# Kernel optimization log

Measured on AMD Instinct MI355X. Metric: run time of the kernel, lower is better.

The kernel has to match this reference:

```python
import jax, jax.numpy as jnp
import numpy as np

B, T, V, H, L = 32, 256, 32000, 512, 2

def setup_inputs() -> dict:
    key = jax.random.key(0)
    ks = jax.random.split(key, 6)
    scale = 1.0 / np.sqrt(H)
    tokens = jax.random.randint(ks[0], (B, T), 0, V)
    lengths = jax.random.randint(ks[1], (B,), T // 2, T + 1)
    embedding = jax.random.normal(ks[2], (V, H), jnp.float32) * scale
    Wx = jax.random.normal(ks[3], (L, H, 4 * H), jnp.float32) * scale
    Wh = jax.random.normal(ks[4], (L, H, 4 * H), jnp.float32) * scale
    b = jnp.zeros((L, 4 * H), jnp.float32)
    return {"tokens": tokens, "lengths": lengths, "embedding": embedding,
            "Wx": Wx, "Wh": Wh, "b": b}

def _lstm_layer(x, lengths, Wx, Wh, b):
    # x: [B, T, H]; length-masked carry (state frozen once t >= length)
    Bb, Tt, Hh = x.shape
    def step(carry, inp):
        c, h = carry
        xt, t = inp
        z = xt @ Wx + h @ Wh + b            # [B, 4H]
        i, f, g, o = jnp.split(z, 4, axis=-1)
        nc = jax.nn.sigmoid(f) * c + jax.nn.sigmoid(i) * jnp.tanh(g)
        nh = jax.nn.sigmoid(o) * jnp.tanh(nc)
        mask = (t < lengths)[:, None]
        c = jnp.where(mask, nc, c)
        h = jnp.where(mask, nh, h)
        return (c, h), h
    init = (jnp.zeros((Bb, Hh), x.dtype), jnp.zeros((Bb, Hh), x.dtype))
    (c, h), ys = jax.lax.scan(step, init, (jnp.swapaxes(x, 0, 1), jnp.arange(Tt)))
    return jnp.swapaxes(ys, 0, 1), (c, h)  # [B, T, H], ([B,H],[B,H])

def reference(tokens, lengths, embedding, Wx, Wh, b):
    x = embedding[tokens]                    # [B, T, H]
    final = None
    for l in range(Wx.shape[0]):             # small fixed layer loop
        x, final = _lstm_layer(x, lengths, Wx[l], Wh[l], b[l])
    # encoder returns (all outputs of top layer, final state of top layer)
    return x, final
```

## Files before the change

kernel.cpp:

```cpp
#include <hip/hip_runtime.h>

#define BB 32
#define TT 256
#define HH 512
#define NBLK 64
#define ALD 1032
#define ZLD 68
#define FLGSTRIDE 32

typedef float    f32x4 __attribute__((ext_vector_type(4)));
typedef float    f32x2 __attribute__((ext_vector_type(2)));
typedef int      i32x4 __attribute__((ext_vector_type(4)));
typedef _Float16 f16x8 __attribute__((ext_vector_type(8)));
typedef unsigned long long u64;

__device__ __forceinline__ unsigned short f2h(float f) {
  union { _Float16 h; unsigned short u; } v; v.h = (_Float16)f; return v.u;
}
__device__ __forceinline__ int pkh2(float a, float b) {
  return (int)((unsigned int)f2h(a) | ((unsigned int)f2h(b) << 16));
}
__device__ __forceinline__ float sigm(float x) { return 1.f / (1.f + __expf(-x)); }
__device__ __forceinline__ float tanh_(float x) {
  float ax = fabsf(x);
  float e = __expf(-2.f * ax);
  float r = (1.f - e) / (1.f + e);
  return copysignf(r, x);
}
__device__ __forceinline__ void ld_coh16(i32x4& dst, const void* a) {
  asm volatile("global_load_dwordx4 %0, %1, off sc1"
               : "=v"(dst) : "v"(a) : "memory");
}

__global__ void zero_ws_kernel(unsigned int* p, int nwords) {
  int i = blockIdx.x * 256 + threadIdx.x;
  if (i < nwords) p[i] = 0u;
}

__global__ __launch_bounds__(256, 1) void lstm_enc_kernel(
    const int* __restrict__ tokens,
    const int* __restrict__ lengths,
    const float* __restrict__ emb,
    const float* __restrict__ Wx,
    const float* __restrict__ Wh,
    const float* __restrict__ bias,
    float* __restrict__ out,
    unsigned short* __restrict__ ws_y,
    u64* __restrict__ htag,
    unsigned int* __restrict__ flags)
{
  const int tid   = threadIdx.x;
  const int blk   = blockIdx.x;
  const int layer = blk >> 5;
  const int lblk  = blk & 31;
  const int wave  = tid >> 6;
  const int lane  = tid & 63;

  __shared__ unsigned short Alds[32 * ALD];
  __shared__ float zlds[32 * ZLD];

  const int nloc  = lane & 15;
  const int gcol  = wave * HH + lblk * 16 + nloc;
  const int krow0 = (lane >> 4) * 8;
  const float* WxL = Wx + (size_t)layer * HH * 2048;
  const float* WhL = Wh + (size_t)layer * HH * 2048;
  f16x8 breg[32];
#pragma unroll
  for (int s = 0; s < 32; ++s) {
    const float* base = (s < 16)
        ? (WxL + (size_t)(s * 32 + krow0) * 2048 + gcol)
        : (WhL + (size_t)((s - 16) * 32 + krow0) * 2048 + gcol);
    f16x8 v;
    v[0] = (_Float16)base[0 * 2048];
    v[1] = (_Float16)base[1 * 2048];
    v[2] = (_Float16)base[2 * 2048];
    v[3] = (_Float16)base[3 * 2048];
    v[4] = (_Float16)base[4 * 2048];
    v[5] = (_Float16)base[5 * 2048];
    v[6] = (_Float16)base[6 * 2048];
    v[7] = (_Float16)base[7 * 2048];
    breg[s] = v;
  }

  const int jj  = tid & 7;
  const int eb  = tid >> 3;
  const int u0  = lblk * 16 + 2 * jj;
  const int len = lengths[eb];
  const float bI0 = bias[layer * 2048 +         u0], bI1 = bias[layer * 2048 +         u0 + 1];
  const float bF0 = bias[layer * 2048 +  512 +  u0], bF1 = bias[layer * 2048 +  512 +  u0 + 1];
  const float bG0 = bias[layer * 2048 + 1024 +  u0], bG1 = bias[layer * 2048 + 1024 +  u0 + 1];
  const float bO0 = bias[layer * 2048 + 1536 +  u0], bO1 = bias[layer * 2048 + 1536 +  u0 + 1];
  float cA = 0.f, hA = 0.f, cB = 0.f, hB = 0.f;

  u64* hlay = htag + (size_t)layer * 2 * BB * 256;
  unsigned int* pollL0 = flags + (size_t)(tid & 31) * FLGSTRIDE;

  if (layer == 0) {
#pragma unroll
    for (int i = 0; i < 8; ++i) {
      int u   = tid + i * 256;
      int row = u >> 6;
      int ce  = (u & 63) * 8;
      int tok = tokens[row * TT + 0];
      const float* src = emb + (size_t)tok * HH + ce;
      f32x4 lo = *(const f32x4*)src;
      f32x4 hi = *(const f32x4*)(src + 4);
      i32x4 w;
      w[0] = pkh2(lo[0], lo[1]); w[1] = pkh2(lo[2], lo[3]);
      w[2] = pkh2(hi[0], hi[1]); w[3] = pkh2(hi[2], hi[3]);
      *(i32x4*)(&Alds[row * ALD + ce]) = w;
    }
  }

  for (int it = 0;; ++it) {
    const int t = (layer == 0) ? it : (it - 1);
    const bool active = (t >= 0) && (t < TT);

    if (layer == 1 && active) {
      const unsigned int tgt = (unsigned int)(t + 1);
      if (tid < 32) {
        while (__hip_atomic_load(pollL0, __ATOMIC_RELAXED, __HIP_MEMORY_SCOPE_AGENT) < tgt) {
          __builtin_amdgcn_s_sleep(1);
        }
      }
      __syncthreads();
      i32x4 yv[8];
      int yrow[8], yco[8];
#pragma unroll
      for (int k = 0; k < 8; ++k) {
        int g = tid + k * 256;
        yrow[k] = g >> 6;
        yco[k]  = (g & 63) * 8;
        ld_coh16(yv[k], ws_y + ((size_t)yrow[k] * TT + t) * HH + yco[k]);
      }
      asm volatile("s_waitcnt vmcnt(0)" ::: "memory");
      __builtin_amdgcn_sched_barrier(0);
#pragma unroll
      for (int k = 0; k < 8; ++k) {
        *(i32x4*)(&Alds[yrow[k] * ALD + yco[k]]) = yv[k];
      }
    }

    if (active) {
      const u64* hsrc = hlay + (size_t)(t & 1) * BB * 256;
      const unsigned int exp = (unsigned int)t;
      i32x4 hv[16];
      bool ok = false;
      while (!ok) {
#pragma unroll
        for (int k = 0; k < 16; ++k) {
          ld_coh16(hv[k], hsrc + 2 * (tid + k * 256));
        }
        asm volatile("s_waitcnt vmcnt(0)" ::: "memory");
        __builtin_amdgcn_sched_barrier(0);
        ok = true;
#pragma unroll
        for (int k = 0; k < 16; ++k) {
          if ((unsigned int)hv[k][1] != exp) ok = false;
          if ((unsigned int)hv[k][3] != exp) ok = false;
        }
      }
#pragma unroll
      for (int k = 0; k < 16; ++k) {
        int g   = tid + k * 256;
        int row = g >> 7;
        int e   = 4 * (g & 127);
        u64 d = (u64)(unsigned int)hv[k][0] | ((u64)(unsigned int)hv[k][2] << 32);
        *(u64*)(&Alds[row * ALD + 512 + e]) = d;
      }
    }
    __syncthreads();

    if (active) {
      f32x4 acc0 = {0.f, 0.f, 0.f, 0.f};
      f32x4 acc1 = {0.f, 0.f, 0.f, 0.f};
      const _Float16* a0p = (const _Float16*)&Alds[nloc * ALD + krow0];
      const _Float16* a1p = a0p + 16 * ALD;
#pragma unroll
      for (int s = 0; s < 32; ++s) {
        f16x8 a0 = *(const f16x8*)(a0p + s * 32);
        f16x8 a1 = *(const f16x8*)(a1p + s * 32);
        acc0 = __builtin_amdgcn_mfma_f32_16x16x32_f16(a0, breg[s], acc0, 0, 0, 0);
        acc1 = __builtin_amdgcn_mfma_f32_16x16x32_f16(a1, breg[s], acc1, 0, 0, 0);
      }
      const int zc = wave * 16 + nloc;
      const int zr = (lane >> 4) * 4;
#pragma unroll
      for (int r = 0; r < 4; ++r) {
        zlds[(zr + r) * ZLD + zc]        = acc0[r];
        zlds[(16 + zr + r) * ZLD + zc]   = acc1[r];
      }
    }
    __syncthreads();

    if (active) {
      float zi0 = zlds[eb * ZLD +      2 * jj] + bI0, zi1 = zlds[eb * ZLD +      2 * jj + 1] + bI1;
      float zf0 = zlds[eb * ZLD + 16 + 2 * jj] + bF0, zf1 = zlds[eb * ZLD + 16 + 2 * jj + 1] + bF1;
      float zg0 = zlds[eb * ZLD + 32 + 2 * jj] + bG0, zg1 = zlds[eb * ZLD + 32 + 2 * jj + 1] + bG1;
      float zo0 = zlds[eb * ZLD + 48 + 2 * jj] + bO0, zo1 = zlds[eb * ZLD + 48 + 2 * jj + 1] + bO1;
      float ncA = sigm(zf0) * cA + sigm(zi0) * tanh_(zg0);
      float nhA = sigm(zo0) * tanh_(ncA);
      float ncB = sigm(zf1) * cB + sigm(zi1) * tanh_(zg1);
      float nhB = sigm(zo1) * tanh_(ncB);
      if (t < len) { cA = ncA; hA = nhA; cB = ncB; hB = nhB; }
      unsigned int hp = (unsigned int)f2h(hA) | ((unsigned int)f2h(hB) << 16);
      u64 hv2 = ((u64)(unsigned int)(t + 1) << 32) | (u64)hp;
      __hip_atomic_store(&hlay[(size_t)((t + 1) & 1) * BB * 256 + eb * 256 + lblk * 8 + jj],
                         hv2, __ATOMIC_RELAXED, __HIP_MEMORY_SCOPE_AGENT);
      if (layer == 0) {
        __hip_atomic_store((unsigned int*)(ws_y + ((size_t)eb * TT + t) * HH + u0), hp,
                           __ATOMIC_RELAXED, __HIP_MEMORY_SCOPE_AGENT);
      } else {
        f32x2 o; o[0] = hA; o[1] = hB;
        *(f32x2*)(out + ((size_t)eb * TT + t) * HH + u0) = o;
      }
    }

    if (it == TT) break;

    if (layer == 0) {
      __syncthreads();
      if (tid == 0 && active) {
        __hip_atomic_store(flags + (size_t)lblk * FLGSTRIDE, (unsigned int)(it + 1),
                           __ATOMIC_RELAXED, __HIP_MEMORY_SCOPE_AGENT);
      }
      const int tn = it + 1;
      if (tn < TT) {
#pragma unroll
        for (int i = 0; i < 8; ++i) {
          int u   = tid + i * 256;
          int row = u >> 6;
          int ce  = (u & 63) * 8;
          int tok = tokens[row * TT + tn];
          const float* src = emb + (size_t)tok * HH + ce;
          f32x4 lo = *(const f32x4*)src;
          f32x4 hi = *(const f32x4*)(src + 4);
          i32x4 w;
          w[0] = pkh2(lo[0], lo[1]); w[1] = pkh2(lo[2], lo[3]);
          w[2] = pkh2(hi[0], hi[1]); w[3] = pkh2(hi[2], hi[3]);
          *(i32x4*)(&Alds[row * ALD + ce]) = w;
        }
      }
    }
  }

  if (layer == 1) {
    const size_t coff = (size_t)BB * TT * HH;
    const size_t hoff = coff + (size_t)BB * HH;
    f32x2 c2; c2[0] = cA; c2[1] = cB;
    f32x2 h2; h2[0] = hA; h2[1] = hB;
    *(f32x2*)(out + coff + (size_t)eb * HH + u0) = c2;
    *(f32x2*)(out + hoff + (size_t)eb * HH + u0) = h2;
  }
}

extern "C" void kernel_launch(void* const* d_in, const int* in_sizes, int n_in,
                              void* d_out, int out_size, void* d_ws, size_t ws_size,
                              hipStream_t stream) {
  (void)in_sizes; (void)n_in; (void)out_size; (void)ws_size;
  const int* tokens  = (const int*)d_in[0];
  const int* lengths = (const int*)d_in[1];
  const float* emb   = (const float*)d_in[2];
  const float* Wx    = (const float*)d_in[3];
  const float* Wh    = (const float*)d_in[4];
  const float* bias  = (const float*)d_in[5];

  char* w = (char*)d_ws;
  const size_t FB = (size_t)32 * FLGSTRIDE * 4;
  const size_t HT = (size_t)2 * 2 * BB * 256 * 8;
  unsigned int*   flags = (unsigned int*)w;
  u64*            htag  = (u64*)(w + FB);
  unsigned short* ws_y  = (unsigned short*)(w + FB + HT);

  const int zero_words = (int)((FB + HT) / 4);
  hipLaunchKernelGGL(zero_ws_kernel, dim3((zero_words + 255) / 256), dim3(256), 0, stream,
                     (unsigned int*)d_ws, zero_words);
  hipLaunchKernelGGL(lstm_enc_kernel, dim3(NBLK), dim3(256), 0, stream,
                     tokens, lengths, emb, Wx, Wh, bias, (float*)d_out,
                     ws_y, htag, flags);
}
```

Baseline: 1.655 ms.

## Place each LSTM layer's blocks on one XCD and poll hidden state via local L2

The kernel now launches 512 blocks. Each block reads its XCC ID and claims a role only if it sits on one of two chosen home XCDs, so each layer's 32 blocks share an L2, and the surplus blocks exit. The per-step hidden-state exchange is written both to an L2-local buffer (plain store) and a device-coherent buffer. Consumers poll the local copy with sc0 loads and fall back to the coherent copy after 48 failed rounds. The goal is to avoid cross-die coherence latency on the serial recurrence, at the cost of more launch overhead, a role-assignment handshake, and reliance on L2 visibility semantics that the fallback only partly guards.

```diff
diff --git a/kernel.cpp b/kernel.cpp
--- a/kernel.cpp
+++ b/kernel.cpp
@@ -3,10 +3,10 @@
 #define BB 32
 #define TT 256
 #define HH 512
-#define NBLK 64
 #define ALD 1032
 #define ZLD 68
 #define FLGSTRIDE 32
+#define GRIDN 512
 
 typedef float    f32x4 __attribute__((ext_vector_type(4)));
 typedef float    f32x2 __attribute__((ext_vector_type(2)));
@@ -28,8 +28,13 @@
   return copysignf(r, x);
 }
 __device__ __forceinline__ void ld_coh16(i32x4& dst, const void* a) {
-  asm volatile("global_load_dwordx4 %0, %1, off sc1"
-               : "=v"(dst) : "v"(a) : "memory");
+  asm volatile("global_load_dwordx4 %0, %1, off sc1" : "=v"(dst) : "v"(a) : "memory");
+}
+__device__ __forceinline__ void ld_l2_16(i32x4& dst, const void* a) {
+  asm volatile("global_load_dwordx4 %0, %1, off sc0" : "=v"(dst) : "v"(a) : "memory");
+}
+__device__ __forceinline__ void st_l2_8(void* a, u64 v) {
+  asm volatile("global_store_dwordx2 %0, %1, off" :: "v"(a), "v"(v) : "memory");
 }
 
 __global__ void zero_ws_kernel(unsigned int* p, int nwords) {
@@ -46,13 +51,56 @@
     const float* __restrict__ bias,
     float* __restrict__ out,
     unsigned short* __restrict__ ws_y,
-    u64* __restrict__ htag,
-    unsigned int* __restrict__ flags)
+    u64* __restrict__ htagL,
+    u64* __restrict__ htagG,
+    unsigned int* __restrict__ flags,
+    unsigned int* __restrict__ ctl)
 {
-  const int tid   = threadIdx.x;
-  const int blk   = blockIdx.x;
-  const int layer = blk >> 5;
-  const int lblk  = blk & 31;
+  const int tid = threadIdx.x;
+
+  __shared__ int sRole;
+  if (tid == 0) {
+    unsigned int xcc;
+    asm volatile("s_getreg_b32 %0, hwreg(HW_REG_XCC_ID)" : "=s"(xcc));
+    xcc &= 7u;
+    if (blockIdx.x == 0) {
+      __hip_atomic_store(&ctl[0], 0x100u | xcc, __ATOMIC_RELAXED, __HIP_MEMORY_SCOPE_AGENT);
+    }
+    unsigned int hw;
+    while ((((hw = __hip_atomic_load(&ctl[0], __ATOMIC_RELAXED, __HIP_MEMORY_SCOPE_AGENT))) & 0x100u) == 0u) {
+      __builtin_amdgcn_s_sleep(1);
+    }
+    const unsigned int home0 = hw & 7u, home1 = (home0 + 1u) & 7u;
+    int role = -1;
+    if (xcc == home0) {
+      unsigned int i = __hip_atomic_fetch_add(&ctl[32], 1u, __ATOMIC_RELAXED, __HIP_MEMORY_SCOPE_AGENT);
+      if (i < 32u) role = (int)i;
+    } else if (xcc == home1) {
+      unsigned int i = __hip_atomic_fetch_add(&ctl[64], 1u, __ATOMIC_RELAXED, __HIP_MEMORY_SCOPE_AGENT);
+      if (i < 32u) role = 32 + (int)i;
+    }
+    if (role < 0) {
+      unsigned int cl = 0; int spins = 0;
+      while ((cl = __hip_atomic_load(&ctl[96], __ATOMIC_RELAXED, __HIP_MEMORY_SCOPE_AGENT)) < 64u
+             && spins < 20000) { __builtin_amdgcn_s_sleep(2); ++spins; }
+      if (cl < 64u) {
+        unsigned int i = __hip_atomic_fetch_add(&ctl[32], 1u, __ATOMIC_RELAXED, __HIP_MEMORY_SCOPE_AGENT);
+        if (i < 32u) role = (int)i;
+        else {
+          unsigned int j = __hip_atomic_fetch_add(&ctl[64], 1u, __ATOMIC_RELAXED, __HIP_MEMORY_SCOPE_AGENT);
+          if (j < 32u) role = 32 + (int)j;
+        }
+      }
+    }
+    if (role >= 0)
+      __hip_atomic_fetch_add(&ctl[96], 1u, __ATOMIC_RELAXED, __HIP_MEMORY_SCOPE_AGENT);
+    sRole = role;
+  }
+  __syncthreads();
+  const int role = sRole;
+  if (role < 0) return;
+  const int layer = role >> 5;
+  const int lblk  = role & 31;
   const int wave  = tid >> 6;
   const int lane  = tid & 63;
 
@@ -92,8 +140,10 @@
   const float bO0 = bias[layer * 2048 + 1536 +  u0], bO1 = bias[layer * 2048 + 1536 +  u0 + 1];
   float cA = 0.f, hA = 0.f, cB = 0.f, hB = 0.f;
 
-  u64* hlay = htag + (size_t)layer * 2 * BB * 256;
+  u64* hlayL = htagL + (size_t)layer * 2 * BB * 256;
+  u64* hlayG = htagG + (size_t)layer * 2 * BB * 256;
   unsigned int* pollL0 = flags + (size_t)(tid & 31) * FLGSTRIDE;
+  bool useG = false;
 
   if (layer == 0) {
 #pragma unroll
@@ -142,14 +192,19 @@
     }
 
     if (active) {
-      const u64* hsrc = hlay + (size_t)(t & 1) * BB * 256;
+      const u64* srcL = hlayL + (size_t)(t & 1) * BB * 256;
+      const u64* srcG = hlayG + (size_t)(t & 1) * BB * 256;
       const unsigned int exp = (unsigned int)t;
       i32x4 hv[16];
+      int rounds = 0;
       bool ok = false;
       while (!ok) {
-#pragma unroll
-        for (int k = 0; k < 16; ++k) {
-          ld_coh16(hv[k], hsrc + 2 * (tid + k * 256));
+        if (useG) {
+#pragma unroll
+          for (int k = 0; k < 16; ++k) ld_coh16(hv[k], srcG + 2 * (tid + k * 256));
+        } else {
+#pragma unroll
+          for (int k = 0; k < 16; ++k) ld_l2_16(hv[k], srcL + 2 * (tid + k * 256));
         }
         asm volatile("s_waitcnt vmcnt(0)" ::: "memory");
         __builtin_amdgcn_sched_barrier(0);
@@ -159,6 +214,7 @@
           if ((unsigned int)hv[k][1] != exp) ok = false;
           if ((unsigned int)hv[k][3] != exp) ok = false;
         }
+        if (!ok && ++rounds > 48) useG = true;
       }
 #pragma unroll
       for (int k = 0; k < 16; ++k) {
@@ -205,8 +261,9 @@
       if (t < len) { cA = ncA; hA = nhA; cB = ncB; hB = nhB; }
       unsigned int hp = (unsigned int)f2h(hA) | ((unsigned int)f2h(hB) << 16);
       u64 hv2 = ((u64)(unsigned int)(t + 1) << 32) | (u64)hp;
-      __hip_atomic_store(&hlay[(size_t)((t + 1) & 1) * BB * 256 + eb * 256 + lblk * 8 + jj],
-                         hv2, __ATOMIC_RELAXED, __HIP_MEMORY_SCOPE_AGENT);
+      const size_t hoff = (size_t)((t + 1) & 1) * BB * 256 + eb * 256 + lblk * 8 + jj;
+      st_l2_8(&hlayL[hoff], hv2);
+      __hip_atomic_store(&hlayG[hoff], hv2, __ATOMIC_RELAXED, __HIP_MEMORY_SCOPE_AGENT);
       if (layer == 0) {
         __hip_atomic_store((unsigned int*)(ws_y + ((size_t)eb * TT + t) * HH + u0), hp,
                            __ATOMIC_RELAXED, __HIP_MEMORY_SCOPE_AGENT);
@@ -267,15 +324,18 @@
 
   char* w = (char*)d_ws;
   const size_t FB = (size_t)32 * FLGSTRIDE * 4;
+  const size_t CT = 512;
   const size_t HT = (size_t)2 * 2 * BB * 256 * 8;
   unsigned int*   flags = (unsigned int*)w;
-  u64*            htag  = (u64*)(w + FB);
-  unsigned short* ws_y  = (unsigned short*)(w + FB + HT);
-
-  const int zero_words = (int)((FB + HT) / 4);
+  unsigned int*   ctl   = (unsigned int*)(w + FB);
+  u64*            htagL = (u64*)(w + FB + CT);
+  u64*            htagG = (u64*)(w + FB + CT + HT);
+  unsigned short* ws_y  = (unsigned short*)(w + FB + CT + 2 * HT);
+
+  const int zero_words = (int)((FB + CT + 2 * HT) / 4);
   hipLaunchKernelGGL(zero_ws_kernel, dim3((zero_words + 255) / 256), dim3(256), 0, stream,
                      (unsigned int*)d_ws, zero_words);
-  hipLaunchKernelGGL(lstm_enc_kernel, dim3(NBLK), dim3(256), 0, stream,
+  hipLaunchKernelGGL(lstm_enc_kernel, dim3(GRIDN), dim3(256), 0, stream,
                      tokens, lengths, emb, Wx, Wh, bias, (float*)d_out,
-                     ws_y, htag, flags);
-}
+                     ws_y, htagL, htagG, flags, ctl);
+}
```

Result: faster. 1.620 ms (median of 2 runs) (-2.1%).
